# Kernel tuning notes

Measured on AMD Instinct MI355X. Metric: run time of the kernel, lower is better.

Reference implementation:

```python
import jax, jax.numpy as jnp
import numpy as np

B, T_Q, T_K, H = 16, 1024, 1024, 1024


def _linear_params(key, fan_in, fan_out):
    kw, kb = jax.random.split(key)
    bound = 1.0 / np.sqrt(fan_in)
    W = jax.random.uniform(kw, (fan_out, fan_in), jnp.float32, -bound, bound)
    b = jax.random.uniform(kb, (fan_out,), jnp.float32, -bound, bound)
    return W, b


def setup_inputs() -> dict:
    key = jax.random.key(0)
    ks = jax.random.split(key, 6)
    query = jax.random.normal(ks[0], (B, T_Q, H), jnp.float32)
    keys = jax.random.normal(ks[1], (B, T_K, H), jnp.float32)
    values = jax.random.normal(ks[2], (B, T_K, H), jnp.float32)
    Wq, bq = _linear_params(ks[3], H, H)
    Wk, bk = _linear_params(ks[4], H, H)
    Wo, bo = _linear_params(ks[5], H, H)
    return {"query": query, "keys": keys, "values": values,
            "Wq": Wq, "bq": bq, "Wk": Wk, "bk": bk, "Wo": Wo, "bo": bo}


def reference(query, keys, values, Wq, bq, Wk, bk, Wo, bo):
    # Linear projections (torch Linear: x @ W.T + b)
    q = jnp.einsum('bth,oh->bto', query, Wq) + bq   # (B, T_Q, H)
    k = jnp.einsum('bsh,oh->bso', keys, Wk) + bk    # (B, T_K, H)
    # Unscaled scores -> softmax over key axis (dropout is identity at eval)
    scores = jnp.einsum('bto,bso->bts', q, k)       # (B, T_Q, T_K)
    attn = jax.nn.softmax(scores, axis=-1)
    ctx = jnp.einsum('bts,bsh->bth', attn, values)  # note: raw values, value_fc unused in source
    ctx = ctx / jnp.sqrt(jnp.float32(values.shape[1]))
    out = jnp.einsum('bth,oh->bto', ctx, Wo) + bo
    return out
```

## Files before the change

kernel.cpp:

```cpp
#include <hip/hip_runtime.h>
#include <math.h>

typedef __attribute__((ext_vector_type(4))) float f32x4;
typedef __attribute__((ext_vector_type(8))) _Float16 h16x8;
typedef __attribute__((ext_vector_type(8))) short s16x8;
typedef __attribute__((ext_vector_type(4))) short s16x4;

__device__ inline unsigned short f2h(float f) {
    union { _Float16 h; unsigned short u; } v; v.h = (_Float16)f; return v.u;
}
__device__ inline float h2f(unsigned short u) {
    union { unsigned short u; _Float16 h; } v; v.u = u; return (float)v.h;
}

__device__ inline void async16(const void* g, void* l) {
    __builtin_amdgcn_global_load_lds(
        (const __attribute__((address_space(1))) unsigned int*)g,
        (__attribute__((address_space(3))) unsigned int*)l, 16, 0, 0);
}

__device__ inline void xcd_swizzle(int& bx, int& by, int& bz) {
    const long gx = gridDim.x, gy = gridDim.y;
    const long nwg = gx * gy * (long)gridDim.z;
    const long hw  = ((long)blockIdx.z * gy + blockIdx.y) * gx + blockIdx.x;
    const long qq = nwg >> 3, rr = nwg & 7;
    const long xcd = hw & 7, pos = hw >> 3;
    const long lg = (xcd < rr) ? xcd * (qq + 1) + pos
                               : rr * (qq + 1) + (xcd - rr) * qq + pos;
    bx = (int)(lg % gx);
    const long rem = lg / gx;
    by = (int)(rem % gy);
    bz = (int)(rem / gy);
}

#define BM 256
#define BN 256
#define BK 64
#define NTHREADS 512

__device__ inline void stage_half(const unsigned short* g, int row0, int kel, int pitch,
                                  unsigned ldsbase, char* smem, int tid) {
    const int rl  = tid >> 3;
    const int scb = ((tid & 7) ^ (rl & 7)) << 4;
    char* wb = smem + ldsbase + (unsigned)((tid >> 6) << 10);
#pragma unroll
    for (int s = 0; s < 2; ++s) {
        long off = ((long)(row0 + s * 64 + rl) * pitch + kel) * 2 + scb;
        async16((const char*)g + off, wb + s * 8192);
    }
}

__device__ inline h16x8 ld_frag(const char* smem, unsigned base, int row, int kbyte) {
    unsigned off = base + (unsigned)(row * 128) + (unsigned)(kbyte ^ ((row & 7) << 4));
    return *(const h16x8*)(smem + off);
}

template<int OM>
__global__ __launch_bounds__(NTHREADS, 2)
void gemm256(const unsigned short* __restrict__ A,
             const unsigned short* __restrict__ B,
             const float* __restrict__ bias,
             void* __restrict__ C, int N, int lenK, int pitch,
             long sA, long sB, long sC, long sBias, float scale)
{
    __shared__ __align__(16) char smem[131072];

    const int tid  = threadIdx.x;
    const int wv   = tid >> 6;
    const int lane = tid & 63;
    const int wr = wv >> 2, wc = wv & 3;
    const int lrow = lane & 15;
    const int kq16 = (lane >> 4) * 16;

    int bx, by, bz; xcd_swizzle(bx, by, bz);
    const int n0 = bx * BN;
    const int m0 = by * BM;

    const unsigned short* Ag = A + (long)bz * sA;
    const unsigned short* Bg = B + (long)bz * sB;
    const int NT = lenK / BK;

    auto stageA = [&](int t, int h) {
        stage_half(Ag, m0 + h * 128, t * BK, pitch,
                   (unsigned)(((t & 1) << 16) + (h << 14)), smem, tid);
    };
    auto stageB = [&](int t, int h) {
        stage_half(Bg, n0 + h * 128, t * BK, pitch,
                   (unsigned)(((t & 1) << 16) + 32768 + (h << 14)), smem, tid);
    };

    f32x4 acc[8][4];
#pragma unroll
    for (int i = 0; i < 8; ++i)
#pragma unroll
        for (int j = 0; j < 4; ++j) acc[i][j] = (f32x4){0.f, 0.f, 0.f, 0.f};

    const unsigned AbaseW = (unsigned)(wr * 16384);
    const unsigned BbaseW = (unsigned)(32768 + (wc >> 1) * 16384);
    const int brow0 = (wc & 1) * 64;

    stageB(0, 0); stageB(0, 1); stageA(0, 0); stageA(0, 1); stageB(1, 0); stageB(1, 1);
    asm volatile("s_waitcnt vmcnt(4)" ::: "memory");
    __builtin_amdgcn_s_barrier();

    h16x8 bfr[4][2], afr[2][2];

    for (int i = 0; i < NT / 2; ++i) {
        const int t1 = 2 * i + 1, t2 = 2 * i + 2, t3 = 2 * i + 3;
#pragma unroll
        for (int half = 0; half < 2; ++half) {
            const unsigned hb = half ? 65536u : 0u;
#pragma unroll
            for (int q = 0; q < 4; ++q) {
                if (q == 0) {
#pragma unroll
                    for (int j = 0; j < 4; ++j)
#pragma unroll
                        for (int ks = 0; ks < 2; ++ks)
                            bfr[j][ks] = ld_frag(smem, hb + BbaseW, brow0 + j * 16 + lrow, ks * 64 + kq16);
                }
#pragma unroll
                for (int f = 0; f < 2; ++f)
#pragma unroll
                    for (int ks = 0; ks < 2; ++ks)
                        afr[f][ks] = ld_frag(smem, hb + AbaseW, q * 32 + f * 16 + lrow, ks * 64 + kq16);
                if (half == 0) {
                    if (q == 0)      stageA(t1, 0);
                    else if (q == 1) stageA(t1, 1);
                    else if (q == 2) { if (t2 < NT) stageB(t2, 0); }
                    else             { if (t2 < NT) stageB(t2, 1); }
                } else {
                    if (q == 0)      { if (t2 < NT) stageA(t2, 0); }
                    else if (q == 1) { if (t2 < NT) stageA(t2, 1); }
                    else if (q == 2) { if (t3 < NT) stageB(t3, 0); }
                    else             { if (t3 < NT) stageB(t3, 1); }
                }

                __builtin_amdgcn_s_barrier();
                asm volatile("s_waitcnt lgkmcnt(0)" ::: "memory");
                __builtin_amdgcn_sched_barrier(0);
                __builtin_amdgcn_s_setprio(1);
#pragma unroll
                for (int ks = 0; ks < 2; ++ks)
#pragma unroll
                    for (int f = 0; f < 2; ++f)
#pragma unroll
                        for (int j = 0; j < 4; ++j)
                            acc[2 * q + f][j] = __builtin_amdgcn_mfma_f32_16x16x32_f16(
                                afr[f][ks], bfr[j][ks], acc[2 * q + f][j], 0, 0, 0);
                __builtin_amdgcn_s_setprio(0);
                if (q == 3) {
                    const int tn = half ? t3 : t2;
                    if (tn < NT) { asm volatile("s_waitcnt vmcnt(4)" ::: "memory"); }
                    else         { asm volatile("s_waitcnt vmcnt(0)" ::: "memory"); }
                }
                __builtin_amdgcn_s_barrier();
            }
        }
    }

#pragma unroll
    for (int j = 0; j < 4; ++j) {
        const int col = n0 + wc * 64 + j * 16 + lrow;
        const float bb = bias ? bias[(long)bz * sBias + col] : 0.f;
#pragma unroll
        for (int mi = 0; mi < 8; ++mi) {
#pragma unroll
            for (int r = 0; r < 4; ++r) {
                const long row = m0 + wr * 128 + mi * 16 + (lane >> 4) * 4 + r;
                const float v = acc[mi][j][r] * scale + bb;
                const long idx = (long)bz * sC + row * (long)N + col;
                if constexpr (OM == 0) ((float*)C)[idx] = v;
                else                   ((unsigned short*)C)[idx] = f2h(v);
            }
        }
    }
}

#define BM2 128
#define BN2 256
#define BK2 32

__device__ inline h16x8 ld_frag32(const char* smem, unsigned base, int row, int kbyte) {
    unsigned off = base + (unsigned)(row * 64) + (unsigned)(kbyte ^ ((row & 3) << 4));
    return *(const h16x8*)(smem + off);
}

template<int OM>
__global__ __launch_bounds__(512, 4)
void gemm128(const unsigned short* __restrict__ A,
             const unsigned short* __restrict__ B,
             const float* __restrict__ bias,
             void* __restrict__ C, int N, int lenK, int pitch,
             long sA, long sB, long sC, long sBias, float scale)
{
    __shared__ __align__(16) char smem[49152];

    const int tid  = threadIdx.x;
    const int wv   = tid >> 6;
    const int lane = tid & 63;
    const int wr = wv >> 2, wc = wv & 3;
    const int lrow = lane & 15;
    const int kq16 = (lane >> 4) * 16;

    int bx, by, bz; xcd_swizzle(bx, by, bz);
    const int n0 = bx * BN2;
    const int m0 = by * BM2;

    const unsigned short* Ag = A + (long)bz * sA;
    const unsigned short* Bg = B + (long)bz * sB;
    const int NT = lenK / BK2;

    auto stage = [&](int t) {
        const unsigned db = (unsigned)((t & 1) * 24576);
        {
            int r = tid >> 2, s = tid & 3, ss = s ^ (r & 3);
            async16((const char*)Ag + ((long)(m0 + r) * pitch + t * BK2 + ss * 8) * 2,
                    smem + db + (unsigned)(wv << 10));
        }
#pragma unroll
        for (int l = 0; l < 2; ++l) {
            int idx = l * 512 + tid;
            int r = idx >> 2, s = idx & 3, ss = s ^ (r & 3);
            async16((const char*)Bg + ((long)(n0 + r) * pitch + t * BK2 + ss * 8) * 2,
                    smem + db + 8192u + (unsigned)(l * 8192) + (unsigned)(wv << 10));
        }
    };

    f32x4 acc[4][4];
#pragma unroll
    for (int i = 0; i < 4; ++i)
#pragma unroll
        for (int j = 0; j < 4; ++j) acc[i][j] = (f32x4){0.f, 0.f, 0.f, 0.f};

    const unsigned Abase = (unsigned)(wr * 4096);
    const unsigned Bbase = 8192u + (unsigned)(wc * 4096);

    stage(0);
    __syncthreads();

#pragma unroll 2
    for (int t = 0; t < NT; ++t) {
        const unsigned db = (unsigned)((t & 1) * 24576);
        if (t + 1 < NT) stage(t + 1);
        h16x8 afr[4], bfr[4];
#pragma unroll
        for (int f = 0; f < 4; ++f) {
            afr[f] = ld_frag32(smem, db + Abase, f * 16 + lrow, kq16);
            bfr[f] = ld_frag32(smem, db + Bbase, f * 16 + lrow, kq16);
        }
#pragma unroll
        for (int mi = 0; mi < 4; ++mi)
#pragma unroll
            for (int j = 0; j < 4; ++j)
                acc[mi][j] = __builtin_amdgcn_mfma_f32_16x16x32_f16(
                    afr[mi], bfr[j], acc[mi][j], 0, 0, 0);
        __syncthreads();
    }

#pragma unroll
    for (int j = 0; j < 4; ++j) {
        const int col = n0 + wc * 64 + j * 16 + lrow;
        const float bb = bias ? bias[(long)bz * sBias + col] : 0.f;
#pragma unroll
        for (int mi = 0; mi < 4; ++mi) {
#pragma unroll
            for (int r = 0; r < 4; ++r) {
                const long row = m0 + wr * 64 + mi * 16 + (lane >> 4) * 4 + r;
                const float v = acc[mi][j][r] * scale + bb;
                const long idx = (long)bz * sC + row * (long)N + col;
                if constexpr (OM == 0) ((float*)C)[idx] = v;
                else                   ((unsigned short*)C)[idx] = f2h(v);
            }
        }
    }
}


__global__ __launch_bounds__(256)
void conv2_f16(const float* __restrict__ a, const float* __restrict__ b,
               unsigned short* __restrict__ oa, unsigned short* __restrict__ ob, int n)
{
    int i = (blockIdx.x * 256 + threadIdx.x) * 4;
    if (i >= n) return;
    const float* in = blockIdx.y ? b : a;
    unsigned short* out = blockIdx.y ? ob : oa;
    float4 v = *(const float4*)(in + i);
    s16x4 o = {(short)f2h(v.x), (short)f2h(v.y), (short)f2h(v.z), (short)f2h(v.w)};
    *(s16x4*)(out + i) = o;
}

__global__ __launch_bounds__(256)
void conv_f16(const float* __restrict__ in, unsigned short* __restrict__ out, int n)
{
    int i = (blockIdx.x * 256 + threadIdx.x) * 4;
    if (i >= n) return;
    float4 v = *(const float4*)(in + i);
    s16x4 o = {(short)f2h(v.x), (short)f2h(v.y), (short)f2h(v.z), (short)f2h(v.w)};
    *(s16x4*)(out + i) = o;
}

__global__ __launch_bounds__(256)
void transpose_f16(const float* __restrict__ in, unsigned short* __restrict__ out)
{
    __shared__ float tile[32][33];
    const long base = (long)blockIdx.z * 1024 * 1024;
    const int h0 = blockIdx.x * 32, t0 = blockIdx.y * 32;
    for (int i = threadIdx.y; i < 32; i += 8)
        tile[i][threadIdx.x] = in[base + (long)(t0 + i) * 1024 + h0 + threadIdx.x];
    __syncthreads();
    for (int i = threadIdx.y; i < 32; i += 8)
        out[base + (long)(h0 + i) * 1024 + t0 + threadIdx.x] = f2h(tile[threadIdx.x][i]);
}

__global__ __launch_bounds__(256)
void transpose2_f16(const float* __restrict__ inA, const float* __restrict__ inB,
                    unsigned short* __restrict__ outA, unsigned short* __restrict__ outB)
{
    __shared__ float tile[32][33];
    const float* in = blockIdx.z ? inB : inA;
    unsigned short* out = blockIdx.z ? outB : outA;
    const int h0 = blockIdx.x * 32, t0 = blockIdx.y * 32;
    for (int i = threadIdx.y; i < 32; i += 8)
        tile[i][threadIdx.x] = in[(long)(t0 + i) * 1024 + h0 + threadIdx.x];
    __syncthreads();
    for (int i = threadIdx.y; i < 32; i += 8)
        out[(long)(h0 + i) * 1024 + t0 + threadIdx.x] = f2h(tile[threadIdx.x][i]);
}

__global__ __launch_bounds__(256)
void w2_kernel(const float* __restrict__ Wk, const float* __restrict__ bq,
               float* __restrict__ w2)
{
    __shared__ float part[4][64];
    const int tx = threadIdx.x & 63;
    const int ty = threadIdx.x >> 6;
    const int h  = blockIdx.x * 64 + tx;
    float s = 0.f;
    for (int o = ty * 256; o < ty * 256 + 256; ++o)
        s = fmaf(Wk[(long)o * 1024 + h], bq[o], s);
    part[ty][tx] = s;
    __syncthreads();
    if (ty == 0) w2[h] = part[0][tx] + part[1][tx] + part[2][tx] + part[3][tx];
}

__global__ __launch_bounds__(256)
void matvec_v(const unsigned short* __restrict__ Xk, const float* __restrict__ w2,
              float* __restrict__ v)
{
    const int wave = threadIdx.x >> 6, lane = threadIdx.x & 63;
    const long row = (long)blockIdx.x * 4 + wave;
    const unsigned short* p = Xk + row * 1024 + lane * 16;
    float s = 0.f;
#pragma unroll
    for (int c = 0; c < 2; ++c) {
        s16x8 hv = *(const s16x8*)(p + c * 8);
#pragma unroll
        for (int e = 0; e < 8; ++e)
            s = fmaf(h2f((unsigned short)hv[e]), w2[lane * 16 + c * 8 + e], s);
    }
#pragma unroll
    for (int off = 1; off < 64; off <<= 1) s += __shfl_xor(s, off);
    if (lane == 0) v[row] = s;
}

__global__ __launch_bounds__(256)
void reduce4(const float* __restrict__ p, unsigned short* __restrict__ MT)
{
    const long i = ((long)blockIdx.x * 256 + threadIdx.x) * 4;
    const long S = 1024L * 1024;
    float4 a = *(const float4*)(p + i);
    float4 b = *(const float4*)(p + S + i);
    float4 c = *(const float4*)(p + 2 * S + i);
    float4 d = *(const float4*)(p + 3 * S + i);
    s16x4 o = {(short)f2h(a.x + b.x + c.x + d.x), (short)f2h(a.y + b.y + c.y + d.y),
               (short)f2h(a.z + b.z + c.z + d.z), (short)f2h(a.w + b.w + c.w + d.w)};
    *(s16x4*)(MT + i) = o;
}

__global__ __launch_bounds__(256)
void softmax_ip(unsigned short* __restrict__ S)
{
    long row = blockIdx.x;
    const int tid = threadIdx.x;
    s16x4 raw = *(s16x4*)(S + row * 1024 + tid * 4);
    float v0 = h2f((unsigned short)raw[0]), v1 = h2f((unsigned short)raw[1]);
    float v2 = h2f((unsigned short)raw[2]), v3 = h2f((unsigned short)raw[3]);
    float m = fmaxf(fmaxf(v0, v1), fmaxf(v2, v3));
#pragma unroll
    for (int off = 1; off < 64; off <<= 1) m = fmaxf(m, __shfl_xor(m, off));
    __shared__ float redm[4];
    int wave = tid >> 6, lane = tid & 63;
    if (lane == 0) redm[wave] = m;
    __syncthreads();
    m = fmaxf(fmaxf(redm[0], redm[1]), fmaxf(redm[2], redm[3]));

    float e0 = expf(v0 - m), e1 = expf(v1 - m), e2 = expf(v2 - m), e3 = expf(v3 - m);
    float s = e0 + e1 + e2 + e3;
#pragma unroll
    for (int off = 1; off < 64; off <<= 1) s += __shfl_xor(s, off);
    __shared__ float reds[4];
    if (lane == 0) reds[wave] = s;
    __syncthreads();
    s = reds[0] + reds[1] + reds[2] + reds[3];
    float inv = 1.f / s;
    s16x4 o = {(short)f2h(e0 * inv), (short)f2h(e1 * inv),
               (short)f2h(e2 * inv), (short)f2h(e3 * inv)};
    *(s16x4*)(S + row * 1024 + tid * 4) = o;
}

extern "C" void kernel_launch(void* const* d_in, const int* in_sizes, int n_in,
                              void* d_out, int out_size, void* d_ws, size_t ws_size,
                              hipStream_t stream)
{
    const float* query  = (const float*)d_in[0];
    const float* keys   = (const float*)d_in[1];
    const float* values = (const float*)d_in[2];
    const float* Wq     = (const float*)d_in[3];
    const float* bq     = (const float*)d_in[4];
    const float* Wk     = (const float*)d_in[5];
    const float* bk     = (const float*)d_in[6];
    const float* Wo     = (const float*)d_in[7];
    const float* bo     = (const float*)d_in[8];
    (void)bk;

    const int  T = 1024, H = 1024;
    const long NE = 16384L * 1024;
    const long NW = 1024L * 1024;

    size_t need = (size_t)(NE * 4 + NW * 12 + 40960) * sizeof(unsigned short);
    if (ws_size < need) return;

    unsigned short* ws   = (unsigned short*)d_ws;
    unsigned short* Xq   = ws;
    unsigned short* Xk   = Xq + NE;
    unsigned short* vT   = Xk + NE;
    unsigned short* P1   = vT + NE;
    unsigned short* WqT  = P1 + NE;
    unsigned short* WkT  = WqT + NW;
    unsigned short* Woh  = WkT + NW;
    unsigned short* MT   = Woh + NW;
    float*          part = (float*)(MT + NW);
    float*          w2   = (float*)(MT + NW * 9);
    float*          vvec = w2 + 1024;
    unsigned short* sc   = Xq;
    unsigned short* ctx  = P1;

    conv2_f16<<<dim3(16384, 2, 1), 256, 0, stream>>>(query, keys, Xq, Xk, (int)NE);
    transpose2_f16<<<dim3(32, 32, 2), dim3(32, 8), 0, stream>>>(Wq, Wk, WqT, WkT);
    conv_f16<<<1024, 256, 0, stream>>>(Wo, Woh, (int)NW);
    transpose_f16<<<dim3(32, 32, 16), dim3(32, 8), 0, stream>>>(values, vT);
    w2_kernel<<<16, 256, 0, stream>>>(Wk, bq, w2);

    gemm128<0><<<dim3(4, 8, 4), 512, 0, stream>>>(
        WkT, WqT, nullptr, part, 1024, 256, 1024, 256, 256, (long)NW, 0, 1.f);
    reduce4<<<1024, 256, 0, stream>>>(part, MT);

    gemm128<1><<<dim3(4, 128, 1), 512, 0, stream>>>(
        Xq, MT, nullptr, P1, H, H, H, 0, 0, 0, 0, 1.f);

    matvec_v<<<4096, 256, 0, stream>>>(Xk, w2, vvec);

    gemm256<1><<<dim3(4, 4, 16), NTHREADS, 0, stream>>>(
        P1, Xk, vvec, sc, T, H, H,
        (long)T * H, (long)T * H, (long)T * T, (long)T, 1.f);

    softmax_ip<<<16384, 256, 0, stream>>>(sc);

    gemm256<1><<<dim3(4, 4, 16), NTHREADS, 0, stream>>>(
        sc, vT, nullptr, ctx, H, T, T,
        (long)T * T, (long)T * H, (long)T * H, 0, 1.f / 32.f);

    gemm128<0><<<dim3(4, 128, 1), 512, 0, stream>>>(
        ctx, Woh, bo, d_out, H, H, H, 0, 0, 0, 0, 1.f);
}
```

Before: 300.1 us.

## Replace 256-tile batched GEMMs with gemm128, grid-stride conversion and wave-per-row softmax

The two batched attention GEMMs (scores and context) now use the existing 128x256-tile gemm128 kernel in place of the 256x256 gemm256, which is deleted. The float-to-half conversion becomes a grid-stride loop handling 16 elements per thread, the values transpose loops over batches inside fewer blocks, and softmax processes one row per wave using only shuffles, with no LDS or block barriers. The aim is better occupancy and load balance on the batched GEMMs and lower launch and synchronisation overhead in the elementwise kernels. The smaller GEMM tile may lower per-block data reuse and raise global traffic.

New measurement: 294.0 us. -2.0%, faster.

```diff
diff --git a/kernel.cpp b/kernel.cpp
--- a/kernel.cpp
+++ b/kernel.cpp
@@ -33,150 +33,6 @@
     bz = (int)(rem / gy);
 }
 
-#define BM 256
-#define BN 256
-#define BK 64
-#define NTHREADS 512
-
-__device__ inline void stage_half(const unsigned short* g, int row0, int kel, int pitch,
-                                  unsigned ldsbase, char* smem, int tid) {
-    const int rl  = tid >> 3;
-    const int scb = ((tid & 7) ^ (rl & 7)) << 4;
-    char* wb = smem + ldsbase + (unsigned)((tid >> 6) << 10);
-#pragma unroll
-    for (int s = 0; s < 2; ++s) {
-        long off = ((long)(row0 + s * 64 + rl) * pitch + kel) * 2 + scb;
-        async16((const char*)g + off, wb + s * 8192);
-    }
-}
-
-__device__ inline h16x8 ld_frag(const char* smem, unsigned base, int row, int kbyte) {
-    unsigned off = base + (unsigned)(row * 128) + (unsigned)(kbyte ^ ((row & 7) << 4));
-    return *(const h16x8*)(smem + off);
-}
-
-template<int OM>
-__global__ __launch_bounds__(NTHREADS, 2)
-void gemm256(const unsigned short* __restrict__ A,
-             const unsigned short* __restrict__ B,
-             const float* __restrict__ bias,
-             void* __restrict__ C, int N, int lenK, int pitch,
-             long sA, long sB, long sC, long sBias, float scale)
-{
-    __shared__ __align__(16) char smem[131072];
-
-    const int tid  = threadIdx.x;
-    const int wv   = tid >> 6;
-    const int lane = tid & 63;
-    const int wr = wv >> 2, wc = wv & 3;
-    const int lrow = lane & 15;
-    const int kq16 = (lane >> 4) * 16;
-
-    int bx, by, bz; xcd_swizzle(bx, by, bz);
-    const int n0 = bx * BN;
-    const int m0 = by * BM;
-
-    const unsigned short* Ag = A + (long)bz * sA;
-    const unsigned short* Bg = B + (long)bz * sB;
-    const int NT = lenK / BK;
-
-    auto stageA = [&](int t, int h) {
-        stage_half(Ag, m0 + h * 128, t * BK, pitch,
-                   (unsigned)(((t & 1) << 16) + (h << 14)), smem, tid);
-    };
-    auto stageB = [&](int t, int h) {
-        stage_half(Bg, n0 + h * 128, t * BK, pitch,
-                   (unsigned)(((t & 1) << 16) + 32768 + (h << 14)), smem, tid);
-    };
-
-    f32x4 acc[8][4];
-#pragma unroll
-    for (int i = 0; i < 8; ++i)
-#pragma unroll
-        for (int j = 0; j < 4; ++j) acc[i][j] = (f32x4){0.f, 0.f, 0.f, 0.f};
-
-    const unsigned AbaseW = (unsigned)(wr * 16384);
-    const unsigned BbaseW = (unsigned)(32768 + (wc >> 1) * 16384);
-    const int brow0 = (wc & 1) * 64;
-
-    stageB(0, 0); stageB(0, 1); stageA(0, 0); stageA(0, 1); stageB(1, 0); stageB(1, 1);
-    asm volatile("s_waitcnt vmcnt(4)" ::: "memory");
-    __builtin_amdgcn_s_barrier();
-
-    h16x8 bfr[4][2], afr[2][2];
-
-    for (int i = 0; i < NT / 2; ++i) {
-        const int t1 = 2 * i + 1, t2 = 2 * i + 2, t3 = 2 * i + 3;
-#pragma unroll
-        for (int half = 0; half < 2; ++half) {
-            const unsigned hb = half ? 65536u : 0u;
-#pragma unroll
-            for (int q = 0; q < 4; ++q) {
-                if (q == 0) {
-#pragma unroll
-                    for (int j = 0; j < 4; ++j)
-#pragma unroll
-                        for (int ks = 0; ks < 2; ++ks)
-                            bfr[j][ks] = ld_frag(smem, hb + BbaseW, brow0 + j * 16 + lrow, ks * 64 + kq16);
-                }
-#pragma unroll
-                for (int f = 0; f < 2; ++f)
-#pragma unroll
-                    for (int ks = 0; ks < 2; ++ks)
-                        afr[f][ks] = ld_frag(smem, hb + AbaseW, q * 32 + f * 16 + lrow, ks * 64 + kq16);
-                if (half == 0) {
-                    if (q == 0)      stageA(t1, 0);
-                    else if (q == 1) stageA(t1, 1);
-                    else if (q == 2) { if (t2 < NT) stageB(t2, 0); }
-                    else             { if (t2 < NT) stageB(t2, 1); }
-                } else {
-                    if (q == 0)      { if (t2 < NT) stageA(t2, 0); }
-                    else if (q == 1) { if (t2 < NT) stageA(t2, 1); }
-                    else if (q == 2) { if (t3 < NT) stageB(t3, 0); }
-                    else             { if (t3 < NT) stageB(t3, 1); }
-                }
-
-                __builtin_amdgcn_s_barrier();
-                asm volatile("s_waitcnt lgkmcnt(0)" ::: "memory");
-                __builtin_amdgcn_sched_barrier(0);
-                __builtin_amdgcn_s_setprio(1);
-#pragma unroll
-                for (int ks = 0; ks < 2; ++ks)
-#pragma unroll
-                    for (int f = 0; f < 2; ++f)
-#pragma unroll
-                        for (int j = 0; j < 4; ++j)
-                            acc[2 * q + f][j] = __builtin_amdgcn_mfma_f32_16x16x32_f16(
-                                afr[f][ks], bfr[j][ks], acc[2 * q + f][j], 0, 0, 0);
-                __builtin_amdgcn_s_setprio(0);
-                if (q == 3) {
-                    const int tn = half ? t3 : t2;
-                    if (tn < NT) { asm volatile("s_waitcnt vmcnt(4)" ::: "memory"); }
-                    else         { asm volatile("s_waitcnt vmcnt(0)" ::: "memory"); }
-                }
-                __builtin_amdgcn_s_barrier();
-            }
-        }
-    }
-
-#pragma unroll
-    for (int j = 0; j < 4; ++j) {
-        const int col = n0 + wc * 64 + j * 16 + lrow;
-        const float bb = bias ? bias[(long)bz * sBias + col] : 0.f;
-#pragma unroll
-        for (int mi = 0; mi < 8; ++mi) {
-#pragma unroll
-            for (int r = 0; r < 4; ++r) {
-                const long row = m0 + wr * 128 + mi * 16 + (lane >> 4) * 4 + r;
-                const float v = acc[mi][j][r] * scale + bb;
-                const long idx = (long)bz * sC + row * (long)N + col;
-                if constexpr (OM == 0) ((float*)C)[idx] = v;
-                else                   ((unsigned short*)C)[idx] = f2h(v);
-            }
-        }
-    }
-}
-
 #define BM2 128
 #define BN2 256
 #define BK2 32
@@ -279,15 +135,34 @@
 
 __global__ __launch_bounds__(256)
 void conv2_f16(const float* __restrict__ a, const float* __restrict__ b,
-               unsigned short* __restrict__ oa, unsigned short* __restrict__ ob, int n)
-{
-    int i = (blockIdx.x * 256 + threadIdx.x) * 4;
-    if (i >= n) return;
-    const float* in = blockIdx.y ? b : a;
-    unsigned short* out = blockIdx.y ? ob : oa;
-    float4 v = *(const float4*)(in + i);
-    s16x4 o = {(short)f2h(v.x), (short)f2h(v.y), (short)f2h(v.z), (short)f2h(v.w)};
-    *(s16x4*)(out + i) = o;
+               unsigned short* __restrict__ oa, unsigned short* __restrict__ ob, long n)
+{
+    const long stride = (long)gridDim.x * 256 * 16;
+    const long t0 = ((long)blockIdx.x * 256 + threadIdx.x) * 16;
+    for (long i = t0; i < n; i += stride) {
+        float4 v0 = *(const float4*)(a + i);
+        float4 v1 = *(const float4*)(a + i + 4);
+        float4 v2 = *(const float4*)(a + i + 8);
+        float4 v3 = *(const float4*)(a + i + 12);
+        s16x8 o0 = {(short)f2h(v0.x), (short)f2h(v0.y), (short)f2h(v0.z), (short)f2h(v0.w),
+                    (short)f2h(v1.x), (short)f2h(v1.y), (short)f2h(v1.z), (short)f2h(v1.w)};
+        s16x8 o1 = {(short)f2h(v2.x), (short)f2h(v2.y), (short)f2h(v2.z), (short)f2h(v2.w),
+                    (short)f2h(v3.x), (short)f2h(v3.y), (short)f2h(v3.z), (short)f2h(v3.w)};
+        *(s16x8*)(oa + i)     = o0;
+        *(s16x8*)(oa + i + 8) = o1;
+    }
+    for (long i = t0; i < n; i += stride) {
+        float4 v0 = *(const float4*)(b + i);
+        float4 v1 = *(const float4*)(b + i + 4);
+        float4 v2 = *(const float4*)(b + i + 8);
+        float4 v3 = *(const float4*)(b + i + 12);
+        s16x8 o0 = {(short)f2h(v0.x), (short)f2h(v0.y), (short)f2h(v0.z), (short)f2h(v0.w),
+                    (short)f2h(v1.x), (short)f2h(v1.y), (short)f2h(v1.z), (short)f2h(v1.w)};
+        s16x8 o1 = {(short)f2h(v2.x), (short)f2h(v2.y), (short)f2h(v2.z), (short)f2h(v2.w),
+                    (short)f2h(v3.x), (short)f2h(v3.y), (short)f2h(v3.z), (short)f2h(v3.w)};
+        *(s16x8*)(ob + i)     = o0;
+        *(s16x8*)(ob + i + 8) = o1;
+    }
 }
 
 __global__ __launch_bounds__(256)
@@ -301,16 +176,19 @@
 }
 
 __global__ __launch_bounds__(256)
-void transpose_f16(const float* __restrict__ in, unsigned short* __restrict__ out)
+void transpose_vals(const float* __restrict__ in, unsigned short* __restrict__ out)
 {
     __shared__ float tile[32][33];
-    const long base = (long)blockIdx.z * 1024 * 1024;
     const int h0 = blockIdx.x * 32, t0 = blockIdx.y * 32;
-    for (int i = threadIdx.y; i < 32; i += 8)
-        tile[i][threadIdx.x] = in[base + (long)(t0 + i) * 1024 + h0 + threadIdx.x];
-    __syncthreads();
-    for (int i = threadIdx.y; i < 32; i += 8)
-        out[base + (long)(h0 + i) * 1024 + t0 + threadIdx.x] = f2h(tile[threadIdx.x][i]);
+    for (int z = blockIdx.z; z < 16; z += gridDim.z) {
+        const long base = (long)z * 1024 * 1024;
+        __syncthreads();
+        for (int i = threadIdx.y; i < 32; i += 8)
+            tile[i][threadIdx.x] = in[base + (long)(t0 + i) * 1024 + h0 + threadIdx.x];
+        __syncthreads();
+        for (int i = threadIdx.y; i < 32; i += 8)
+            out[base + (long)(h0 + i) * 1024 + t0 + threadIdx.x] = f2h(tile[threadIdx.x][i]);
+    }
 }
 
 __global__ __launch_bounds__(256)
@@ -379,34 +257,40 @@
 }
 
 __global__ __launch_bounds__(256)
-void softmax_ip(unsigned short* __restrict__ S)
-{
-    long row = blockIdx.x;
-    const int tid = threadIdx.x;
-    s16x4 raw = *(s16x4*)(S + row * 1024 + tid * 4);
-    float v0 = h2f((unsigned short)raw[0]), v1 = h2f((unsigned short)raw[1]);
-    float v2 = h2f((unsigned short)raw[2]), v3 = h2f((unsigned short)raw[3]);
-    float m = fmaxf(fmaxf(v0, v1), fmaxf(v2, v3));
-#pragma unroll
-    for (int off = 1; off < 64; off <<= 1) m = fmaxf(m, __shfl_xor(m, off));
-    __shared__ float redm[4];
-    int wave = tid >> 6, lane = tid & 63;
-    if (lane == 0) redm[wave] = m;
-    __syncthreads();
-    m = fmaxf(fmaxf(redm[0], redm[1]), fmaxf(redm[2], redm[3]));
-
-    float e0 = expf(v0 - m), e1 = expf(v1 - m), e2 = expf(v2 - m), e3 = expf(v3 - m);
-    float s = e0 + e1 + e2 + e3;
-#pragma unroll
-    for (int off = 1; off < 64; off <<= 1) s += __shfl_xor(s, off);
-    __shared__ float reds[4];
-    if (lane == 0) reds[wave] = s;
-    __syncthreads();
-    s = reds[0] + reds[1] + reds[2] + reds[3];
-    float inv = 1.f / s;
-    s16x4 o = {(short)f2h(e0 * inv), (short)f2h(e1 * inv),
-               (short)f2h(e2 * inv), (short)f2h(e3 * inv)};
-    *(s16x4*)(S + row * 1024 + tid * 4) = o;
+void softmax_wave(unsigned short* __restrict__ S)
+{
+    const int wave = threadIdx.x >> 6, lane = threadIdx.x & 63;
+    for (long row = (long)blockIdx.x * 4 + wave; row < 16384; row += (long)gridDim.x * 4) {
+        unsigned short* p = S + row * 1024;
+        s16x8 ra = *(s16x8*)(p + lane * 8);
+        s16x8 rb = *(s16x8*)(p + 512 + lane * 8);
+        float va[8], vb[8];
+        float m = -3.0e38f;
+#pragma unroll
+        for (int e = 0; e < 8; ++e) {
+            va[e] = h2f((unsigned short)ra[e]); m = fmaxf(m, va[e]);
+            vb[e] = h2f((unsigned short)rb[e]); m = fmaxf(m, vb[e]);
+        }
+#pragma unroll
+        for (int off = 1; off < 64; off <<= 1) m = fmaxf(m, __shfl_xor(m, off));
+        float s = 0.f;
+#pragma unroll
+        for (int e = 0; e < 8; ++e) {
+            va[e] = expf(va[e] - m); s += va[e];
+            vb[e] = expf(vb[e] - m); s += vb[e];
+        }
+#pragma unroll
+        for (int off = 1; off < 64; off <<= 1) s += __shfl_xor(s, off);
+        const float inv = 1.f / s;
+        s16x8 oa, ob;
+#pragma unroll
+        for (int e = 0; e < 8; ++e) {
+            oa[e] = (short)f2h(va[e] * inv);
+            ob[e] = (short)f2h(vb[e] * inv);
+        }
+        *(s16x8*)(p + lane * 8)       = oa;
+        *(s16x8*)(p + 512 + lane * 8) = ob;
+    }
 }
 
 extern "C" void kernel_launch(void* const* d_in, const int* in_sizes, int n_in,
@@ -446,10 +330,10 @@
     unsigned short* sc   = Xq;
     unsigned short* ctx  = P1;
 
-    conv2_f16<<<dim3(16384, 2, 1), 256, 0, stream>>>(query, keys, Xq, Xk, (int)NE);
+    conv2_f16<<<2048, 256, 0, stream>>>(query, keys, Xq, Xk, NE);
     transpose2_f16<<<dim3(32, 32, 2), dim3(32, 8), 0, stream>>>(Wq, Wk, WqT, WkT);
     conv_f16<<<1024, 256, 0, stream>>>(Wo, Woh, (int)NW);
-    transpose_f16<<<dim3(32, 32, 16), dim3(32, 8), 0, stream>>>(values, vT);
+    transpose_vals<<<dim3(32, 32, 4), dim3(32, 8), 0, stream>>>(values, vT);
     w2_kernel<<<16, 256, 0, stream>>>(Wk, bq, w2);
 
     gemm128<0><<<dim3(4, 8, 4), 512, 0, stream>>>(
@@ -461,13 +345,13 @@
 
     matvec_v<<<4096, 256, 0, stream>>>(Xk, w2, vvec);
 
-    gemm256<1><<<dim3(4, 4, 16), NTHREADS, 0, stream>>>(
+    gemm128<1><<<dim3(4, 8, 16), 512, 0, stream>>>(
         P1, Xk, vvec, sc, T, H, H,
         (long)T * H, (long)T * H, (long)T * T, (long)T, 1.f);
 
-    softmax_ip<<<16384, 256, 0, stream>>>(sc);
-
-    gemm256<1><<<dim3(4, 4, 16), NTHREADS, 0, stream>>>(
+    softmax_wave<<<2048, 256, 0, stream>>>(sc);
+
+    gemm128<1><<<dim3(4, 8, 16), 512, 0, stream>>>(
         sc, vT, nullptr, ctx, H, T, T,
         (long)T * T, (long)T * H, (long)T * H, 0, 1.f / 32.f);
 
```
